# Performance work log

Measured on AMD Instinct MI355X. Metric: run time of the kernel, lower is better.

## Reference

```python
import jax, jax.numpy as jnp
import numpy as np

B, C1, C2, K, H, W = 2, 256, 256, 3, 64, 64
PAD = 1
EPS = 1e-5
K2 = K * K
OUT_OFF = 3 * K2  # deform_groups=1: 2*k2 offset channels + k2 mask channels


def setup_inputs() -> dict:
    key = jax.random.key(0)
    ks = jax.random.split(key, 8)
    x = jax.random.normal(ks[0], (B, C1, H, W), jnp.float32)
    # small scale so predicted offsets stay within a few pixels (realistic trained regime)
    w_off = jax.random.normal(ks[1], (OUT_OFF, C1, 3, 3), jnp.float32) * 0.01
    b_off = jax.random.normal(ks[2], (OUT_OFF,), jnp.float32) * 0.01
    w_dcn = jax.random.normal(ks[3], (C2, C1, K, K), jnp.float32) / np.sqrt(C1 * K2).astype(np.float32)
    gamma = 1.0 + 0.1 * jax.random.normal(ks[4], (C2,), jnp.float32)
    beta = 0.1 * jax.random.normal(ks[5], (C2,), jnp.float32)
    run_mean = 0.1 * jax.random.normal(ks[6], (C2,), jnp.float32)
    run_var = jax.random.uniform(ks[7], (C2,), jnp.float32, minval=0.5, maxval=1.5)
    return {"x": x, "w_off": w_off, "b_off": b_off, "w_dcn": w_dcn,
            "gamma": gamma, "beta": beta, "run_mean": run_mean, "run_var": run_var}


def _dcnv2_bn_silu(x, w_off, b_off, w_dcn, gamma, beta, run_mean, run_var):
    # offset/mask predictor: plain 3x3 conv, stride 1, pad 1
    om = jax.lax.conv_general_dilated(x, w_off, (1, 1), [(PAD, PAD), (PAD, PAD)])
    om = om + b_off[None, :, None, None]  # [B, 27, H, W]
    # mmcv channel layout: (dy, dx) interleaved per kernel tap, then mask
    offset = om[:, :2 * K2].reshape(B, K2, 2, H, W)
    mask = jax.nn.sigmoid(om[:, 2 * K2:3 * K2])  # [B, K2, H, W]
    dy, dx = offset[:, :, 0], offset[:, :, 1]     # [B, K2, H, W]

    ki = jnp.arange(K)
    tap_y = jnp.repeat(ki, K)  # [K2]
    tap_x = jnp.tile(ki, K)    # [K2]
    base_y = jnp.arange(H)[None, None, :, None] - PAD + tap_y[None, :, None, None]
    base_x = jnp.arange(W)[None, None, None, :] - PAD + tap_x[None, :, None, None]
    py = base_y.astype(x.dtype) + dy  # [B, K2, H, W] sampling rows
    px = base_x.astype(x.dtype) + dx  # [B, K2, H, W] sampling cols

    y0f = jnp.floor(py)
    x0f = jnp.floor(px)
    ly = (py - y0f)[:, None]  # [B, 1, K2, H, W]
    lx = (px - x0f)[:, None]
    y0 = y0f.astype(jnp.int32)
    x0 = x0f.astype(jnp.int32)

    x_flat = x.reshape(B, C1, H * W)

    def gather(yi, xi):
        valid = ((yi >= 0) & (yi < H) & (xi >= 0) & (xi < W)).astype(x.dtype)
        idx = jnp.clip(yi, 0, H - 1) * W + jnp.clip(xi, 0, W - 1)  # [B, K2, H, W]
        v = jnp.take_along_axis(x_flat, idx.reshape(B, 1, -1), axis=2)
        return v.reshape(B, C1, K2, H, W) * valid[:, None]

    v00 = gather(y0, x0)
    v01 = gather(y0, x0 + 1)
    v10 = gather(y0 + 1, x0)
    v11 = gather(y0 + 1, x0 + 1)
    vals = (v00 * (1 - ly) * (1 - lx) + v01 * (1 - ly) * lx
            + v10 * ly * (1 - lx) + v11 * ly * lx)
    vals = vals * mask[:, None]  # modulated

    out = jnp.einsum('bckhw,ock->bohw', vals, w_dcn.reshape(C2, C1, K2))

    # BatchNorm (inference, running stats) + SiLU
    inv = gamma / jnp.sqrt(run_var + EPS)
    y = out * inv[None, :, None, None] + (beta - run_mean * inv)[None, :, None, None]
    return y * jax.nn.sigmoid(y)


def reference(x, w_off, b_off, w_dcn, gamma, beta, run_mean, run_var):
    return _dcnv2_bn_silu(x, w_off, b_off, w_dcn, gamma, beta, run_mean, run_var)
```

## Files before the change

kernel.cpp:

```cpp
#include <hip/hip_runtime.h>
#include <hip/hip_bf16.h>
#include <math.h>

typedef __bf16 bf16x8 __attribute__((ext_vector_type(8)));
typedef float  f32x4  __attribute__((ext_vector_type(4)));

#define BB 2
#define C1 256
#define C2 256
#define HH 64
#define WW 64
#define HW 4096
#define OCH 27
#define EPSV 1e-5f

#define WBF_OFF  0u
#define WOFF_OFF 1179648u
#define XT_OFF   1327104u

__global__ __launch_bounds__(256) void prep_kernel(
    const float* __restrict__ x, const float* __restrict__ w_dcn,
    const float* __restrict__ w_off, __bf16* __restrict__ xT,
    __bf16* __restrict__ wbfS, __bf16* __restrict__ woffS)
{
    __shared__ __bf16 tile[64][72];
    __shared__ __bf16 lw[16][584];
    const int bi = blockIdx.x, tid = threadIdx.x;

    if (bi < 512) {
        const int b = bi >> 8;
        const int ht = (bi & 255) >> 2;
        const int ct = bi & 3;
        const int hw_l = tid & 63, cg = tid >> 6;
        const float* src = x + ((size_t)(b * 256 + ct * 64 + cg * 16) << 12)
                             + ht * 64 + hw_l;
        #pragma unroll
        for (int i = 0; i < 16; i++)
            tile[hw_l][cg * 16 + i] = (__bf16)src[(size_t)i << 12];
        __syncthreads();
        const int hw_o = tid >> 2, cq = tid & 3;
        __bf16* dst = xT + ((size_t)(b * HW + ht * 64 + hw_o) << 8)
                         + ct * 64 + cq * 16;
        *(bf16x8*)dst       = *(const bf16x8*)&tile[hw_o][cq * 16];
        *(bf16x8*)(dst + 8) = *(const bf16x8*)&tile[hw_o][cq * 16 + 8];
    } else if (bi < 576) {
        const int b2 = bi - 512;
        const int nb = b2 >> 2, qtr = b2 & 3;
        #pragma unroll
        for (int ii = 0; ii < 9; ii++) {
            int m = tid + 256 * ii;
            int base = m * 4;
            int o_l = base / 576;
            int f = base - o_l * 576;
            float4 v = *(const float4*)(w_dcn
                + (size_t)(nb * 16 + o_l) * 2304 + qtr * 576 + f);
            lw[o_l][f]     = (__bf16)v.x;
            lw[o_l][f + 1] = (__bf16)v.y;
            lw[o_l][f + 2] = (__bf16)v.z;
            lw[o_l][f + 3] = (__bf16)v.w;
        }
        __syncthreads();
        #pragma unroll
        for (int ii = 0; ii < 36; ii++) {
            int e = ii * 256 + tid;
            int seg = e >> 9, s = e & 511;
            int lane = s >> 3, j = s & 7;
            int tap = seg >> 1, ks = seg & 1;
            int kb = tap * 4 + qtr;
            int o_l = lane & 15, kq = (lane >> 4) & 3;
            int c_local = ks * 32 + kq * 8 + j;
            wbfS[((size_t)(((kb * 2 + ks) * 16 + nb) * 64 + lane)) * 8 + j]
                = lw[o_l][c_local * 9 + tap];
        }
    } else {
        int t = (bi - 576) * 256 + tid;
        int l = t & 63;
        int nf = (t >> 6) & 1;
        int ks = (t >> 7) & 1;
        int kb = t >> 8;
        int o = nf * 16 + (l & 15);
        int kq = (l >> 4) & 3;
        bf16x8 v;
        #pragma unroll
        for (int j = 0; j < 8; j++) {
            int K = kb * 64 + ks * 32 + kq * 8 + j;
            v[j] = (o < OCH) ? (__bf16)w_off[o * 2304 + (K & 255) * 9 + (K >> 8)]
                             : (__bf16)0.f;
        }
        *(bf16x8*)(woffS + (size_t)t * 8) = v;
    }
}

union SU {
    float sD[4][16][33];
    float sC[2][16][260];
};

__global__ __launch_bounds__(256) void fused_kernel(
    const __bf16* __restrict__ xT, const __bf16* __restrict__ wbfS,
    const __bf16* __restrict__ woffS, const float* __restrict__ b_off,
    const float* __restrict__ gamma, const float* __restrict__ beta,
    const float* __restrict__ rmean, const float* __restrict__ rvar,
    float* __restrict__ out)
{
    __shared__ SU u;
    __shared__ float  sOm[32][16];
    __shared__ int4   sO[9][16];
    __shared__ float4 sW[9][16];

    const int tid = threadIdx.x, wv = tid >> 6, lane = tid & 63;
    const int g = (blockIdx.x & 7) * 64 + (blockIdx.x >> 3);
    const int pixBase = g * 16;
    const int b = pixBase >> 12;
    const int hwBase = pixBase & 4095;
    const int h = hwBase >> 6, w0 = hwBase & 63;
    const int n15 = lane & 15, q4 = lane >> 4;

    const char* xb = (const char*)xT + ((size_t)b << 12) * 512;

    {
        f32x4 acc2[2];
        #pragma unroll
        for (int j = 0; j < 2; j++) acc2[j] = (f32x4){0.f, 0.f, 0.f, 0.f};

        for (int i = 0; i < 9; i++) {
            const int kb = wv * 9 + i;
            const int k = kb >> 2, cc = kb & 3;
            const int kh = k / 3, kw = k % 3;
            const int hh = h + kh - 1;
            const int ww = w0 + n15 + kw - 1;
            const bool valid = (hh >= 0) && (hh < HH) && (ww >= 0) && (ww < WW);
            const int hc = min(max(hh, 0), HH - 1);
            const int wc = min(max(ww, 0), WW - 1);
            const char* src = xb + (size_t)(hc * WW + wc) * 512
                                 + (cc * 64 + q4 * 8) * 2;
            bf16x8 af[2];
            af[0] = *(const bf16x8*)src;
            af[1] = *(const bf16x8*)(src + 64);
            if (!valid) {
                #pragma unroll
                for (int j = 0; j < 8; j++) {
                    af[0][j] = (__bf16)0.f; af[1][j] = (__bf16)0.f;
                }
            }
            #pragma unroll
            for (int nf = 0; nf < 2; nf++) {
                #pragma unroll
                for (int ks = 0; ks < 2; ks++) {
                    bf16x8 bfr = *(const bf16x8*)(woffS
                        + ((size_t)(((kb * 2 + ks) * 2 + nf) * 64 + lane)) * 8);
                    acc2[nf] = __builtin_amdgcn_mfma_f32_16x16x32_bf16(
                        af[ks], bfr, acc2[nf], 0, 0, 0);
                }
            }
        }
        #pragma unroll
        for (int nf = 0; nf < 2; nf++)
            #pragma unroll
            for (int r = 0; r < 4; r++)
                u.sD[wv][q4 * 4 + r][nf * 16 + n15] = acc2[nf][r];
    }
    __syncthreads();
    for (int t = tid; t < OCH * 16; t += 256) {
        int oc = t >> 4, p = t & 15;
        sOm[oc][p] = b_off[oc] + u.sD[0][p][oc] + u.sD[1][p][oc]
                               + u.sD[2][p][oc] + u.sD[3][p][oc];
    }
    __syncthreads();

    if (tid < 144) {
        int k = tid >> 4, p = tid & 15;
        float dy = sOm[2 * k][p];
        float dx = sOm[2 * k + 1][p];
        float mm = sOm[18 + k][p];
        mm = 1.f / (1.f + __expf(-mm));
        float py = (float)(h - 1 + k / 3) + dy;
        float px = (float)(w0 + p - 1 + k % 3) + dx;
        float y0f = floorf(py), x0f = floorf(px);
        float ly = py - y0f, lx = px - x0f;
        int y0 = (int)y0f, x0 = (int)x0f;
        int yc0 = min(max(y0, 0), HH - 1),     yc1 = min(max(y0 + 1, 0), HH - 1);
        int xc0 = min(max(x0, 0), WW - 1),     xc1 = min(max(x0 + 1, 0), WW - 1);
        float vy0 = (y0 >= 0 && y0 < HH) ? 1.f : 0.f;
        float vy1 = (y0 + 1 >= 0 && y0 + 1 < HH) ? 1.f : 0.f;
        float vx0 = (x0 >= 0 && x0 < WW) ? 1.f : 0.f;
        float vx1 = (x0 + 1 >= 0 && x0 + 1 < WW) ? 1.f : 0.f;
        sO[k][p] = (int4){(yc0 * WW + xc0) * 512, (yc0 * WW + xc1) * 512,
                          (yc1 * WW + xc0) * 512, (yc1 * WW + xc1) * 512};
        sW[k][p] = (float4){(1.f - ly) * (1.f - lx) * vy0 * vx0 * mm,
                            (1.f - ly) * lx         * vy0 * vx1 * mm,
                            ly         * (1.f - lx) * vy1 * vx0 * mm,
                            ly         * lx         * vy1 * vx1 * mm};
    }
    __syncthreads();

    f32x4 acc[16];
    #pragma unroll
    for (int j = 0; j < 16; j++) acc[j] = (f32x4){0.f, 0.f, 0.f, 0.f};

    for (int i = 0; i < 9; i++) {
        const int kb = wv * 9 + i;
        const int k = kb >> 2, cc = kb & 3;
        const int4   O = sO[k][n15];
        const float4 W = sW[k][n15];
        const char* base = xb + (cc * 64 + q4 * 8) * 2;

        bf16x8 af[2];
        #pragma unroll
        for (int ks = 0; ks < 2; ks++) {
            const char* bc = base + ks * 64;
            bf16x8 c00 = *(const bf16x8*)(bc + O.x);
            bf16x8 c01 = *(const bf16x8*)(bc + O.y);
            bf16x8 c10 = *(const bf16x8*)(bc + O.z);
            bf16x8 c11 = *(const bf16x8*)(bc + O.w);
            bf16x8 a;
            #pragma unroll
            for (int j = 0; j < 8; j++) {
                float v = W.x * (float)c00[j] + W.y * (float)c01[j]
                        + W.z * (float)c10[j] + W.w * (float)c11[j];
                a[j] = (__bf16)v;
            }
            af[ks] = a;
        }

        #pragma unroll
        for (int half = 0; half < 2; half++) {
            bf16x8 bfr[8][2];
            #pragma unroll
            for (int nb = 0; nb < 8; nb++)
                #pragma unroll
                for (int ks = 0; ks < 2; ks++)
                    bfr[nb][ks] = *(const bf16x8*)(wbfS
                        + ((size_t)(((kb * 2 + ks) * 16 + half * 8 + nb) * 64 + lane)) * 8);
            #pragma unroll
            for (int nb = 0; nb < 8; nb++)
                #pragma unroll
                for (int ks = 0; ks < 2; ks++)
                    acc[half * 8 + nb] = __builtin_amdgcn_mfma_f32_16x16x32_bf16(
                        af[ks], bfr[nb][ks], acc[half * 8 + nb], 0, 0, 0);
        }
    }

    if (wv < 2) {
        #pragma unroll
        for (int nb = 0; nb < 16; nb++)
            #pragma unroll
            for (int r = 0; r < 4; r++)
                u.sC[wv][q4 * 4 + r][nb * 16 + n15] = acc[nb][r];
    }
    __syncthreads();
    if (wv >= 2) {
        #pragma unroll
        for (int nb = 0; nb < 16; nb++)
            #pragma unroll
            for (int r = 0; r < 4; r++)
                u.sC[wv - 2][q4 * 4 + r][nb * 16 + n15] += acc[nb][r];
    }
    __syncthreads();

    const int px = tid & 15, og = tid >> 4;
    float* ob = out + ((size_t)b * C2 << 12) + hwBase + px;
    #pragma unroll
    for (int ii = 0; ii < 16; ii++) {
        int o = og * 16 + ii;
        float s = u.sC[0][px][o] + u.sC[1][px][o];
        float inv = gamma[o] * rsqrtf(rvar[o] + EPSV);
        float sh = beta[o] - rmean[o] * inv;
        float y = s * inv + sh;
        ob[(size_t)o << 12] = y * (1.f / (1.f + __expf(-y)));
    }
}

extern "C" void kernel_launch(void* const* d_in, const int* in_sizes, int n_in,
                              void* d_out, int out_size, void* d_ws, size_t ws_size,
                              hipStream_t stream) {
    const float* x      = (const float*)d_in[0];
    const float* w_off  = (const float*)d_in[1];
    const float* b_off  = (const float*)d_in[2];
    const float* w_dcn  = (const float*)d_in[3];
    const float* gamma  = (const float*)d_in[4];
    const float* beta   = (const float*)d_in[5];
    const float* rmean  = (const float*)d_in[6];
    const float* rvar   = (const float*)d_in[7];
    float* out = (float*)d_out;

    char* ws = (char*)d_ws;
    __bf16* wbfS  = (__bf16*)(ws + WBF_OFF);
    __bf16* woffS = (__bf16*)(ws + WOFF_OFF);
    __bf16* xT    = (__bf16*)(ws + XT_OFF);

    prep_kernel<<<612, 256, 0, stream>>>(x, w_dcn, w_off, xT, wbfS, woffS);
    fused_kernel<<<512, 256, 0, stream>>>(xT, wbfS, woffS, b_off,
                                          gamma, beta, rmean, rvar, out);
}
```

Before: 122.3 us.

## Double-buffer bilinear corner gathers and vectorize weight repack stores

The main loop now prefetches the four bilinear corner vectors for the next tap into a second register buffer while the current tap is interpolated and fed to MFMA, so global-load latency can hide behind compute. The offset-conv loop and main loop are fully unrolled, and launch bounds request two blocks per SM. The prep kernel's weight repack now writes 8-element bf16 vectors instead of scalar stores. This raises register pressure, which the occupancy hint may force into spills.

```diff
diff --git a/kernel.cpp b/kernel.cpp
--- a/kernel.cpp
+++ b/kernel.cpp
@@ -60,17 +60,17 @@
             lw[o_l][f + 3] = (__bf16)v.w;
         }
         __syncthreads();
-        #pragma unroll
-        for (int ii = 0; ii < 36; ii++) {
-            int e = ii * 256 + tid;
-            int seg = e >> 9, s = e & 511;
-            int lane = s >> 3, j = s & 7;
+        for (int p = tid; p < 1152; p += 256) {
+            int lane = p & 63, seg = p >> 6;
             int tap = seg >> 1, ks = seg & 1;
             int kb = tap * 4 + qtr;
             int o_l = lane & 15, kq = (lane >> 4) & 3;
-            int c_local = ks * 32 + kq * 8 + j;
-            wbfS[((size_t)(((kb * 2 + ks) * 16 + nb) * 64 + lane)) * 8 + j]
-                = lw[o_l][c_local * 9 + tap];
+            bf16x8 v;
+            #pragma unroll
+            for (int j = 0; j < 8; j++)
+                v[j] = lw[o_l][(ks * 32 + kq * 8 + j) * 9 + tap];
+            *(bf16x8*)(wbfS
+                + ((size_t)(((kb * 2 + ks) * 16 + nb) * 64 + lane)) * 8) = v;
         }
     } else {
         int t = (bi - 576) * 256 + tid;
@@ -96,7 +96,7 @@
     float sC[2][16][260];
 };
 
-__global__ __launch_bounds__(256) void fused_kernel(
+__global__ __launch_bounds__(256, 2) void fused_kernel(
     const __bf16* __restrict__ xT, const __bf16* __restrict__ wbfS,
     const __bf16* __restrict__ woffS, const float* __restrict__ b_off,
     const float* __restrict__ gamma, const float* __restrict__ beta,
@@ -123,6 +123,7 @@
         #pragma unroll
         for (int j = 0; j < 2; j++) acc2[j] = (f32x4){0.f, 0.f, 0.f, 0.f};
 
+        #pragma unroll
         for (int i = 0; i < 9; i++) {
             const int kb = wv * 9 + i;
             const int k = kb >> 2, cc = kb & 3;
@@ -198,26 +199,44 @@
     #pragma unroll
     for (int j = 0; j < 16; j++) acc[j] = (f32x4){0.f, 0.f, 0.f, 0.f};
 
+    bf16x8 cor[2][2][4];
+    float4 Wbuf[2];
+
+    auto loadCor = [&](int i, int buf) {
+        const int kb = wv * 9 + i;
+        const int k = kb >> 2, cc = kb & 3;
+        const int4 O = sO[k][n15];
+        Wbuf[buf] = sW[k][n15];
+        const char* base = xb + (cc * 64 + q4 * 8) * 2;
+        #pragma unroll
+        for (int ks = 0; ks < 2; ks++) {
+            const char* bc = base + ks * 64;
+            cor[buf][ks][0] = *(const bf16x8*)(bc + O.x);
+            cor[buf][ks][1] = *(const bf16x8*)(bc + O.y);
+            cor[buf][ks][2] = *(const bf16x8*)(bc + O.z);
+            cor[buf][ks][3] = *(const bf16x8*)(bc + O.w);
+        }
+    };
+
+    loadCor(0, 0);
+    #pragma unroll
     for (int i = 0; i < 9; i++) {
         const int kb = wv * 9 + i;
-        const int k = kb >> 2, cc = kb & 3;
-        const int4   O = sO[k][n15];
-        const float4 W = sW[k][n15];
-        const char* base = xb + (cc * 64 + q4 * 8) * 2;
-
+        const int buf = i & 1;
+
+        if (i < 8) loadCor(i + 1, (i + 1) & 1);
+
+        const float4 W = Wbuf[buf];
         bf16x8 af[2];
         #pragma unroll
         for (int ks = 0; ks < 2; ks++) {
-            const char* bc = base + ks * 64;
-            bf16x8 c00 = *(const bf16x8*)(bc + O.x);
-            bf16x8 c01 = *(const bf16x8*)(bc + O.y);
-            bf16x8 c10 = *(const bf16x8*)(bc + O.z);
-            bf16x8 c11 = *(const bf16x8*)(bc + O.w);
             bf16x8 a;
             #pragma unroll
             for (int j = 0; j < 8; j++) {
-                float v = W.x * (float)c00[j] + W.y * (float)c01[j]
-                        + W.z * (float)c10[j] + W.w * (float)c11[j];
+                float v = W.x * (float)cor[buf][ks][0][j]
+                        + W.y * (float)cor[buf][ks][1][j]
+                        + W.z * (float)cor[buf][ks][2][j]
+                        + W.w * (float)cor[buf][ks][3][j];
                 a[j] = (__bf16)v;
             }
             af[ks] = a;
```

Result: no change. 122.6 us (+0.3%).

## Double pixel tile per block, split K across eight waves, reuse weight fragments

Applied to the files above, without the earlier changes.

The fused kernel now handles 32 pixels per block with 512 threads across 8 waves. Each wave owns 4–5 of the 36 K-blocks and computes two M-fragments, so every loaded weight fragment feeds two MFMAs, halving weight traffic per pixel. The cross-wave reduction and BN+SiLU epilogue now run in four 64-channel passes through shared memory. The prep kernel writes the reordered weights as 8-wide vectors instead of scalars. In exchange the grid is halved to 256 blocks, the K split is uneven across waves, and register pressure rises with 32 accumulators per thread.

```diff
diff --git a/kernel.cpp b/kernel.cpp
--- a/kernel.cpp
+++ b/kernel.cpp
@@ -60,17 +60,17 @@
             lw[o_l][f + 3] = (__bf16)v.w;
         }
         __syncthreads();
-        #pragma unroll
-        for (int ii = 0; ii < 36; ii++) {
-            int e = ii * 256 + tid;
-            int seg = e >> 9, s = e & 511;
-            int lane = s >> 3, j = s & 7;
+        for (int p = tid; p < 1152; p += 256) {
+            int lane = p & 63, seg = p >> 6;
             int tap = seg >> 1, ks = seg & 1;
             int kb = tap * 4 + qtr;
             int o_l = lane & 15, kq = (lane >> 4) & 3;
-            int c_local = ks * 32 + kq * 8 + j;
-            wbfS[((size_t)(((kb * 2 + ks) * 16 + nb) * 64 + lane)) * 8 + j]
-                = lw[o_l][c_local * 9 + tap];
+            bf16x8 v;
+            #pragma unroll
+            for (int j = 0; j < 8; j++)
+                v[j] = lw[o_l][(ks * 32 + kq * 8 + j) * 9 + tap];
+            *(bf16x8*)(wbfS
+                + ((size_t)(((kb * 2 + ks) * 16 + nb) * 64 + lane)) * 8) = v;
         }
     } else {
         int t = (bi - 576) * 256 + tid;
@@ -92,11 +92,11 @@
 }
 
 union SU {
-    float sD[4][16][33];
-    float sC[2][16][260];
+    float sD[8][32][33];
+    float sRed[8][32][68];
 };
 
-__global__ __launch_bounds__(256) void fused_kernel(
+__global__ __launch_bounds__(512, 2) void fused_kernel(
     const __bf16* __restrict__ xT, const __bf16* __restrict__ wbfS,
     const __bf16* __restrict__ woffS, const float* __restrict__ b_off,
     const float* __restrict__ gamma, const float* __restrict__ beta,
@@ -104,13 +104,13 @@
     float* __restrict__ out)
 {
     __shared__ SU u;
-    __shared__ float  sOm[32][16];
-    __shared__ int4   sO[9][16];
-    __shared__ float4 sW[9][16];
+    __shared__ float  sOm[32][32];
+    __shared__ int4   sO[9][32];
+    __shared__ float4 sW[9][32];
 
     const int tid = threadIdx.x, wv = tid >> 6, lane = tid & 63;
-    const int g = (blockIdx.x & 7) * 64 + (blockIdx.x >> 3);
-    const int pixBase = g * 16;
+    const int g = (blockIdx.x & 7) * 32 + (blockIdx.x >> 3);
+    const int pixBase = g * 32;
     const int b = pixBase >> 12;
     const int hwBase = pixBase & 4095;
     const int h = hwBase >> 6, w0 = hwBase & 63;
@@ -118,29 +118,40 @@
 
     const char* xb = (const char*)xT + ((size_t)b << 12) * 512;
 
+    const int kbStart = (wv < 4) ? wv * 5 : 20 + (wv - 4) * 4;
+    const int kbCount = (wv < 4) ? 5 : 4;
+
     {
-        f32x4 acc2[2];
-        #pragma unroll
-        for (int j = 0; j < 2; j++) acc2[j] = (f32x4){0.f, 0.f, 0.f, 0.f};
-
-        for (int i = 0; i < 9; i++) {
-            const int kb = wv * 9 + i;
+        f32x4 acc2[2][2];
+        #pragma unroll
+        for (int i = 0; i < 2; i++)
+            #pragma unroll
+            for (int j = 0; j < 2; j++)
+                acc2[i][j] = (f32x4){0.f, 0.f, 0.f, 0.f};
+
+        for (int ii = 0; ii < kbCount; ii++) {
+            const int kb = kbStart + ii;
             const int k = kb >> 2, cc = kb & 3;
             const int kh = k / 3, kw = k % 3;
             const int hh = h + kh - 1;
-            const int ww = w0 + n15 + kw - 1;
-            const bool valid = (hh >= 0) && (hh < HH) && (ww >= 0) && (ww < WW);
+            const bool vh = (hh >= 0) && (hh < HH);
             const int hc = min(max(hh, 0), HH - 1);
-            const int wc = min(max(ww, 0), WW - 1);
-            const char* src = xb + (size_t)(hc * WW + wc) * 512
-                                 + (cc * 64 + q4 * 8) * 2;
-            bf16x8 af[2];
-            af[0] = *(const bf16x8*)src;
-            af[1] = *(const bf16x8*)(src + 64);
-            if (!valid) {
-                #pragma unroll
-                for (int j = 0; j < 8; j++) {
-                    af[0][j] = (__bf16)0.f; af[1][j] = (__bf16)0.f;
+
+            bf16x8 af[2][2];
+            #pragma unroll
+            for (int mf = 0; mf < 2; mf++) {
+                const int ww = w0 + mf * 16 + n15 + kw - 1;
+                const bool valid = vh && (ww >= 0) && (ww < WW);
+                const int wc = min(max(ww, 0), WW - 1);
+                const char* src = xb + (size_t)(hc * WW + wc) * 512
+                                     + (cc * 64 + q4 * 8) * 2;
+                af[mf][0] = *(const bf16x8*)src;
+                af[mf][1] = *(const bf16x8*)(src + 64);
+                if (!valid) {
+                    #pragma unroll
+                    for (int j = 0; j < 8; j++) {
+                        af[mf][0][j] = (__bf16)0.f; af[mf][1][j] = (__bf16)0.f;
+                    }
                 }
             }
             #pragma unroll
@@ -149,27 +160,33 @@
                 for (int ks = 0; ks < 2; ks++) {
                     bf16x8 bfr = *(const bf16x8*)(woffS
                         + ((size_t)(((kb * 2 + ks) * 2 + nf) * 64 + lane)) * 8);
-                    acc2[nf] = __builtin_amdgcn_mfma_f32_16x16x32_bf16(
-                        af[ks], bfr, acc2[nf], 0, 0, 0);
+                    #pragma unroll
+                    for (int mf = 0; mf < 2; mf++)
+                        acc2[mf][nf] = __builtin_amdgcn_mfma_f32_16x16x32_bf16(
+                            af[mf][ks], bfr, acc2[mf][nf], 0, 0, 0);
                 }
             }
         }
         #pragma unroll
-        for (int nf = 0; nf < 2; nf++)
-            #pragma unroll
-            for (int r = 0; r < 4; r++)
-                u.sD[wv][q4 * 4 + r][nf * 16 + n15] = acc2[nf][r];
+        for (int mf = 0; mf < 2; mf++)
+            #pragma unroll
+            for (int nf = 0; nf < 2; nf++)
+                #pragma unroll
+                for (int r = 0; r < 4; r++)
+                    u.sD[wv][mf * 16 + q4 * 4 + r][nf * 16 + n15] = acc2[mf][nf][r];
     }
     __syncthreads();
-    for (int t = tid; t < OCH * 16; t += 256) {
-        int oc = t >> 4, p = t & 15;
-        sOm[oc][p] = b_off[oc] + u.sD[0][p][oc] + u.sD[1][p][oc]
-                               + u.sD[2][p][oc] + u.sD[3][p][oc];
+    for (int t = tid; t < OCH * 32; t += 512) {
+        int oc = t >> 5, p = t & 31;
+        float s = b_off[oc];
+        #pragma unroll
+        for (int w = 0; w < 8; w++) s += u.sD[w][p][oc];
+        sOm[oc][p] = s;
     }
     __syncthreads();
 
-    if (tid < 144) {
-        int k = tid >> 4, p = tid & 15;
+    if (tid < 288) {
+        int k = tid >> 5, p = tid & 31;
         float dy = sOm[2 * k][p];
         float dx = sOm[2 * k + 1][p];
         float mm = sOm[18 + k][p];
@@ -194,80 +211,87 @@
     }
     __syncthreads();
 
-    f32x4 acc[16];
+    f32x4 acc[2][16];
     #pragma unroll
-    for (int j = 0; j < 16; j++) acc[j] = (f32x4){0.f, 0.f, 0.f, 0.f};
-
-    for (int i = 0; i < 9; i++) {
-        const int kb = wv * 9 + i;
+    for (int i = 0; i < 2; i++)
+        #pragma unroll
+        for (int j = 0; j < 16; j++)
+            acc[i][j] = (f32x4){0.f, 0.f, 0.f, 0.f};
+
+    for (int ii = 0; ii < kbCount; ii++) {
+        const int kb = kbStart + ii;
         const int k = kb >> 2, cc = kb & 3;
-        const int4   O = sO[k][n15];
-        const float4 W = sW[k][n15];
         const char* base = xb + (cc * 64 + q4 * 8) * 2;
 
-        bf16x8 af[2];
-        #pragma unroll
-        for (int ks = 0; ks < 2; ks++) {
-            const char* bc = base + ks * 64;
-            bf16x8 c00 = *(const bf16x8*)(bc + O.x);
-            bf16x8 c01 = *(const bf16x8*)(bc + O.y);
-            bf16x8 c10 = *(const bf16x8*)(bc + O.z);
-            bf16x8 c11 = *(const bf16x8*)(bc + O.w);
-            bf16x8 a;
-            #pragma unroll
-            for (int j = 0; j < 8; j++) {
-                float v = W.x * (float)c00[j] + W.y * (float)c01[j]
-                        + W.z * (float)c10[j] + W.w * (float)c11[j];
-                a[j] = (__bf16)v;
+        bf16x8 af[2][2];
+        #pragma unroll
+        for (int mf = 0; mf < 2; mf++) {
+            const int4   O = sO[k][mf * 16 + n15];
+            const float4 W = sW[k][mf * 16 + n15];
+            #pragma unroll
+            for (int ks = 0; ks < 2; ks++) {
+                const char* bc = base + ks * 64;
+                bf16x8 c00 = *(const bf16x8*)(bc + O.x);
+                bf16x8 c01 = *(const bf16x8*)(bc + O.y);
+                bf16x8 c10 = *(const bf16x8*)(bc + O.z);
+                bf16x8 c11 = *(const bf16x8*)(bc + O.w);
+                bf16x8 a;
+                #pragma unroll
+                for (int j = 0; j < 8; j++) {
+                    float v = W.x * (float)c00[j] + W.y * (float)c01[j]
+                            + W.z * (float)c10[j] + W.w * (float)c11[j];
+                    a[j] = (__bf16)v;
+                }
+                af[mf][ks] = a;
             }
-            af[ks] = a;
-        }
-
-        #pragma unroll
-        for (int half = 0; half < 2; half++) {
-            bf16x8 bfr[8][2];
-            #pragma unroll
-            for (int nb = 0; nb < 8; nb++)
+        }
+
+        #pragma unroll
+        for (int grp = 0; grp < 4; grp++) {
+            bf16x8 bfr[4][2];
+            #pragma unroll
+            for (int nb = 0; nb < 4; nb++)
                 #pragma unroll
                 for (int ks = 0; ks < 2; ks++)
                     bfr[nb][ks] = *(const bf16x8*)(wbfS
-                        + ((size_t)(((kb * 2 + ks) * 16 + half * 8 + nb) * 64 + lane)) * 8);
-            #pragma unroll
-            for (int nb = 0; nb < 8; nb++)
+                        + ((size_t)(((kb * 2 + ks) * 16 + grp * 4 + nb) * 64 + lane)) * 8);
+            #pragma unroll
+            for (int nb = 0; nb < 4; nb++)
                 #pragma unroll
                 for (int ks = 0; ks < 2; ks++)
-                    acc[half * 8 + nb] = __builtin_amdgcn_mfma_f32_16x16x32_bf16(
-                        af[ks], bfr[nb][ks], acc[half * 8 + nb], 0, 0, 0);
-        }
-    }
-
-    if (wv < 2) {
-        #pragma unroll
-        for (int nb = 0; nb < 16; nb++)
-            #pragma unroll
-            for (int r = 0; r < 4; r++)
-                u.sC[wv][q4 * 4 + r][nb * 16 + n15] = acc[nb][r];
-    }
-    __syncthreads();
-    if (wv >= 2) {
-        #pragma unroll
-        for (int nb = 0; nb < 16; nb++)
-            #pragma unroll
-            for (int r = 0; r < 4; r++)
-                u.sC[wv - 2][q4 * 4 + r][nb * 16 + n15] += acc[nb][r];
-    }
-    __syncthreads();
-
-    const int px = tid & 15, og = tid >> 4;
-    float* ob = out + ((size_t)b * C2 << 12) + hwBase + px;
+                    #pragma unroll
+                    for (int mf = 0; mf < 2; mf++)
+                        acc[mf][grp * 4 + nb] = __builtin_amdgcn_mfma_f32_16x16x32_bf16(
+                            af[mf][ks], bfr[nb][ks], acc[mf][grp * 4 + nb], 0, 0, 0);
+        }
+    }
+
     #pragma unroll
-    for (int ii = 0; ii < 16; ii++) {
-        int o = og * 16 + ii;
-        float s = u.sC[0][px][o] + u.sC[1][px][o];
-        float inv = gamma[o] * rsqrtf(rvar[o] + EPSV);
-        float sh = beta[o] - rmean[o] * inv;
-        float y = s * inv + sh;
-        ob[(size_t)o << 12] = y * (1.f / (1.f + __expf(-y)));
+    for (int pass = 0; pass < 4; pass++) {
+        #pragma unroll
+        for (int mf = 0; mf < 2; mf++)
+            #pragma unroll
+            for (int nb = 0; nb < 4; nb++)
+                #pragma unroll
+                for (int r = 0; r < 4; r++)
+                    u.sRed[wv][mf * 16 + q4 * 4 + r][nb * 16 + n15]
+                        = acc[mf][pass * 4 + nb][r];
+        __syncthreads();
+        #pragma unroll
+        for (int t2 = 0; t2 < 4; t2++) {
+            int t = tid + t2 * 512;
+            int px = t & 31, col = t >> 5;
+            float s = 0.f;
+            #pragma unroll
+            for (int w = 0; w < 8; w++) s += u.sRed[w][px][col];
+            int o = pass * 64 + col;
+            float inv = gamma[o] * rsqrtf(rvar[o] + EPSV);
+            float sh = beta[o] - rmean[o] * inv;
+            float y = s * inv + sh;
+            out[(size_t)((b * C2 + o) << 12) + hwBase + px]
+                = y * (1.f / (1.f + __expf(-y)));
+        }
+        __syncthreads();
     }
 }
 
@@ -290,6 +314,6 @@
     __bf16* xT    = (__bf16*)(ws + XT_OFF);
 
     prep_kernel<<<612, 256, 0, stream>>>(x, w_dcn, w_off, xT, wbfS, woffS);
-    fused_kernel<<<512, 256, 0, stream>>>(xT, wbfS, woffS, b_off,
+    fused_kernel<<<256, 512, 0, stream>>>(xT, wbfS, woffS, b_off,
                                           gamma, beta, rmean, rvar, out);
 }
```

Result: no change. 122.0 us (-0.2%).
